# Kernel tuning notes

Measured on AMD Instinct MI355X. Metric: run time of the kernel, lower is better.

The kernel has to match this reference:

```python
import jax, jax.numpy as jnp
import numpy as np


def setup_inputs() -> dict:
    key = jax.random.key(0)
    kq, kk, kv = jax.random.split(key, 3)
    B, H, S, D = 4, 16, 2048, 64
    Q = jax.random.normal(kq, (B, H, S, D), dtype=jnp.float32)
    K = jax.random.normal(kk, (B, H, S, D), dtype=jnp.float32)
    V = jax.random.normal(kv, (B, H, S, D), dtype=jnp.float32)
    return {"Q": Q, "K": K, "V": V}


def reference(Q, K, V):
    # Faithful to the source: scale = d**(-2); scores = (Q @ K^T) / scale
    # i.e. scores are MULTIPLIED by d^2 (quirk of the original module).
    d = K.shape[-1]
    scale = jnp.asarray(d, Q.dtype) ** (-2)
    scores = jnp.einsum('bhqd,bhkd->bhqk', Q, K) / scale  # [B,H,S,S]
    attn = jax.nn.softmax(scores, axis=-1)
    out = jnp.einsum('bhqk,bhkd->bhqd', attn, V)
    return out
```

## Files before the change

kernel.cpp:

```cpp
#include <hip/hip_runtime.h>
#include <math.h>


#define S_LEN 2048
#define D_DIM 64
#define NH 64
#define BM 128
#define BN 64
#define QTILES (S_LEN / BM)
#define KTILES (S_LEN / BN)

typedef unsigned short u16;
typedef unsigned int u32;
typedef _Float16 f16;
typedef __attribute__((ext_vector_type(8))) _Float16 f16x8;
typedef __attribute__((ext_vector_type(4))) float f32x4;

#define SC_FULL (4096.0f * 1.4426950408889634f)
#define QSCALE (SC_FULL / 64.0f)
#define KSCALE 64.0f

union f16cv { f16 h; u16 u; };

__device__ __forceinline__ void split2h(float a, u16& hi, u16& lo) {
  f16cv ch, cl;
  ch.h = (f16)a;
  float r = a - (float)ch.h;
  cl.h = (f16)r;
  hi = ch.u; lo = cl.u;
}

__device__ __forceinline__ int swz(int row, int chunk) {
  return (row << 6) + ((chunk ^ (row & 7)) << 3);
}

__global__ void k_split_kernel(const float* __restrict__ K,
                               u16* __restrict__ Kh, u16* __restrict__ Km) {
  size_t i4 = ((size_t)blockIdx.x * 256 + threadIdx.x) * 4;
  float4 v = *(const float4*)(K + i4);
  u16 h0, l0, h1, l1, h2, l2, h3, l3;
  split2h(v.x * KSCALE, h0, l0);
  split2h(v.y * KSCALE, h1, l1);
  split2h(v.z * KSCALE, h2, l2);
  split2h(v.w * KSCALE, h3, l3);
  *(uint2*)(Kh + i4) = make_uint2((u32)h0 | ((u32)h1 << 16), (u32)h2 | ((u32)h3 << 16));
  *(uint2*)(Km + i4) = make_uint2((u32)l0 | ((u32)l1 << 16), (u32)l2 | ((u32)l3 << 16));
}

__global__ void v_prep_kernel(const float* __restrict__ V, u16* __restrict__ Vt) {
  __shared__ float Vf[64 * 65];
  const int tid = threadIdx.x;
  const int kt = blockIdx.x, h = blockIdx.y;
  const float* V0 = V + ((size_t)h * S_LEN + kt * 64) * 64;
  const int tx = tid & 15, ty = tid >> 4;
#pragma unroll
  for (int p = 0; p < 4; ++p) {
    int r = ty + 16 * p;
    float4 v = *(const float4*)(V0 + r * 64 + tx * 4);
    Vf[r * 65 + 4 * tx + 0] = v.x;
    Vf[r * 65 + 4 * tx + 1] = v.y;
    Vf[r * 65 + 4 * tx + 2] = v.z;
    Vf[r * 65 + 4 * tx + 3] = v.w;
  }
  __syncthreads();
  const int ch = tid & 7, dr = tid >> 3;
#pragma unroll
  for (int p = 0; p < 2; ++p) {
    int d = dr + 32 * p;
    u32 w[4];
#pragma unroll
    for (int i = 0; i < 4; ++i) {
      f16cv a, b;
      a.h = (f16)Vf[(8 * ch + 2 * i) * 65 + d];
      b.h = (f16)Vf[(8 * ch + 2 * i + 1) * 65 + d];
      w[i] = (u32)a.u | ((u32)b.u << 16);
    }
    size_t o = ((size_t)h * 64 + d) * S_LEN + (size_t)kt * 64 + 8 * ch;
    *(uint4*)(Vt + o) = make_uint4(w[0], w[1], w[2], w[3]);
  }
}

#define K0_B 0
#define K1_B 4096
#define VT_B 8192
#define P_B  12288
#define LDS_USH 20480

__global__ __launch_bounds__(512, 4)
void attn_mfma_f16(const float* __restrict__ Q, const u16* __restrict__ Kh,
                   const u16* __restrict__ Km, const u16* __restrict__ Vt,
                   float* __restrict__ O) {
  __shared__ __align__(16) u16 lds[LDS_USH];

  const int tid = threadIdx.x;
  const int lane = tid & 63;
  const int wv = tid >> 6;
  const int c = lane & 15;
  const int g = lane >> 4;
  const int h = blockIdx.x;
  const int qtile = blockIdx.y;

  f16x8 aqh[2], aqm[2];
  {
    int qrow = qtile * BM + wv * 16 + c;
    const float* qp = Q + ((size_t)h * S_LEN + qrow) * 64 + g * 8;
#pragma unroll
    for (int ks = 0; ks < 2; ++ks) {
      float4 a = *(const float4*)(qp + ks * 32);
      float4 b = *(const float4*)(qp + ks * 32 + 4);
      float v[8] = {a.x, a.y, a.z, a.w, b.x, b.y, b.z, b.w};
      f16x8 hi, lo;
#pragma unroll
      for (int e = 0; e < 8; ++e) {
        float q = v[e] * QSCALE;
        f16 qh = (f16)q;
        hi[e] = qh;
        lo[e] = (f16)(q - (float)qh);
      }
      aqh[ks] = hi; aqm[ks] = lo;
    }
  }

  f32x4 Oacc[4];
  f32x4 mrow = (f32x4){-INFINITY, -INFINITY, -INFINITY, -INFINITY};
  f32x4 lrow = (f32x4){0.f, 0.f, 0.f, 0.f};
#pragma unroll
  for (int t = 0; t < 4; ++t) Oacc[t] = (f32x4){0.f, 0.f, 0.f, 0.f};

  const int srow = tid >> 3;
  const int schk = tid & 7;
  const int sdst = swz(srow, schk);
  const size_t gKbase = ((size_t)h * S_LEN) * 64 + (size_t)srow * 64 + schk * 8;
  const size_t gVbase = (size_t)h * 64 * S_LEN + (size_t)srow * S_LEN + schk * 8;

  uint4 rkh, rkm, rvt;
  rkh = *(const uint4*)(Kh + gKbase);
  rkm = *(const uint4*)(Km + gKbase);
  rvt = *(const uint4*)(Vt + gVbase);

  for (int kt = 0; kt < KTILES; ++kt) {
    __syncthreads();
    *(uint4*)&lds[K0_B + sdst] = rkh;
    *(uint4*)&lds[K1_B + sdst] = rkm;
    *(uint4*)&lds[VT_B + sdst] = rvt;
    __syncthreads();

    if (kt + 1 < KTILES) {
      size_t gK = gKbase + (size_t)(kt + 1) * BN * 64;
      size_t gV = gVbase + (size_t)(kt + 1) * BN;
      rkh = *(const uint4*)(Kh + gK);
      rkm = *(const uint4*)(Km + gK);
      rvt = *(const uint4*)(Vt + gV);
    }

    f32x4 S[4];
#pragma unroll
    for (int t = 0; t < 4; ++t) S[t] = (f32x4){0.f, 0.f, 0.f, 0.f};
#pragma unroll
    for (int ks = 0; ks < 2; ++ks) {
#pragma unroll
      for (int t = 0; t < 4; ++t) {
        int off = swz(16 * t + c, g + 4 * ks);
        f16x8 bh = *(const f16x8*)&lds[K0_B + off];
        f16x8 bm = *(const f16x8*)&lds[K1_B + off];
        S[t] = __builtin_amdgcn_mfma_f32_16x16x32_f16(aqh[ks], bh, S[t], 0, 0, 0);
        S[t] = __builtin_amdgcn_mfma_f32_16x16x32_f16(aqh[ks], bm, S[t], 0, 0, 0);
        S[t] = __builtin_amdgcn_mfma_f32_16x16x32_f16(aqm[ks], bh, S[t], 0, 0, 0);
      }
    }

    f32x4 mx;
#pragma unroll
    for (int r = 0; r < 4; ++r)
      mx[r] = fmaxf(fmaxf(S[0][r], S[1][r]), fmaxf(S[2][r], S[3][r]));
#pragma unroll
    for (int r = 0; r < 4; ++r) {
      float v = mx[r];
      v = fmaxf(v, __shfl_xor(v, 1));
      v = fmaxf(v, __shfl_xor(v, 2));
      v = fmaxf(v, __shfl_xor(v, 4));
      v = fmaxf(v, __shfl_xor(v, 8));
      mx[r] = v;
    }
    f32x4 alpha;
#pragma unroll
    for (int r = 0; r < 4; ++r) {
      float mnew = fmaxf(mrow[r], mx[r]);
      alpha[r] = exp2f(mrow[r] - mnew);
      mrow[r] = mnew;
    }
#pragma unroll
    for (int t = 0; t < 4; ++t)
#pragma unroll
      for (int r = 0; r < 4; ++r) S[t][r] = exp2f(S[t][r] - mrow[r]);
#pragma unroll
    for (int r = 0; r < 4; ++r)
      lrow[r] = lrow[r] * alpha[r] + (S[0][r] + S[1][r] + S[2][r] + S[3][r]);
#pragma unroll
    for (int t = 0; t < 4; ++t)
#pragma unroll
      for (int r = 0; r < 4; ++r) Oacc[t][r] *= alpha[r];

#pragma unroll
    for (int r = 0; r < 4; ++r) {
      int rq = wv * 16 + 4 * g + r;
      int rowbase = (rq << 6);
      int rsw = rq & 7;
#pragma unroll
      for (int t = 0; t < 4; ++t) {
        f16cv cv; cv.h = (f16)S[t][r];
        int col = 16 * t + c;
        lds[P_B + rowbase + (((col >> 3) ^ rsw) << 3) + (col & 7)] = cv.u;
      }
    }

    f16x8 ap[2];
    {
      int rq = wv * 16 + c;
#pragma unroll
      for (int ks = 0; ks < 2; ++ks)
        ap[ks] = *(const f16x8*)&lds[P_B + swz(rq, g + 4 * ks)];
    }
#pragma unroll
    for (int ks = 0; ks < 2; ++ks) {
#pragma unroll
      for (int nt = 0; nt < 4; ++nt) {
        f16x8 bv = *(const f16x8*)&lds[VT_B + swz(16 * nt + c, g + 4 * ks)];
        Oacc[nt] = __builtin_amdgcn_mfma_f32_16x16x32_f16(ap[ks], bv, Oacc[nt], 0, 0, 0);
      }
    }
  }

  float inv[4];
#pragma unroll
  for (int r = 0; r < 4; ++r) {
    float l = lrow[r];
    l += __shfl_xor(l, 1);
    l += __shfl_xor(l, 2);
    l += __shfl_xor(l, 4);
    l += __shfl_xor(l, 8);
    inv[r] = 1.0f / l;
  }
#pragma unroll
  for (int nt = 0; nt < 4; ++nt)
#pragma unroll
    for (int r = 0; r < 4; ++r) {
      int row = qtile * BM + wv * 16 + 4 * g + r;
      O[((size_t)h * S_LEN + row) * 64 + 16 * nt + c] = Oacc[nt][r] * inv[r];
    }
}

#define LSTR 68
__global__ __launch_bounds__(256, 2)
void attn_fp32_kernel(const float* __restrict__ Q, const float* __restrict__ K,
                      const float* __restrict__ V, float* __restrict__ O) {
  __shared__ float Qs[64][LSTR];
  __shared__ float Ks[64][LSTR];
  __shared__ float Vs[64][LSTR];
  __shared__ float Ps[64][LSTR];
  const int tid = threadIdx.x;
  const int tx = tid & 15, ty = tid >> 4;
  const int qtile = blockIdx.x, head = blockIdx.y;
  const long hoff = (long)head * S_LEN * D_DIM;
  const float* Qp = Q + hoff + (long)qtile * 64 * D_DIM;
  const float* Kp = K + hoff;
  const float* Vp = V + hoff;
  float* Op = O + hoff + (long)qtile * 64 * D_DIM;
  {
    const int cc = tx * 4;
#pragma unroll
    for (int p = 0; p < 4; ++p) {
      const int r = ty + p * 16;
      *(float4*)(&Qs[r][cc]) = *(const float4*)(Qp + r * D_DIM + cc);
    }
  }
  float m_i[4], l_i[4];
  float4 o_acc[4];
#pragma unroll
  for (int i = 0; i < 4; ++i) {
    m_i[i] = -INFINITY; l_i[i] = 0.0f;
    o_acc[i] = make_float4(0.f, 0.f, 0.f, 0.f);
  }
  const float SCALE = 4096.0f;
  const float LOG2E = 1.4426950408889634f;
  for (int kt = 0; kt < S_LEN / 64; ++kt) {
    {
      const int cc = tx * 4;
      const float* Kt = Kp + kt * 64 * D_DIM;
      const float* Vv = Vp + kt * 64 * D_DIM;
#pragma unroll
      for (int p = 0; p < 4; ++p) {
        const int r = ty + p * 16;
        *(float4*)(&Ks[r][cc]) = *(const float4*)(Kt + r * D_DIM + cc);
        *(float4*)(&Vs[r][cc]) = *(const float4*)(Vv + r * D_DIM + cc);
      }
    }
    __syncthreads();
    float s[4][4];
#pragma unroll
    for (int i = 0; i < 4; ++i)
#pragma unroll
      for (int j = 0; j < 4; ++j) s[i][j] = 0.0f;
#pragma unroll
    for (int d = 0; d < D_DIM; d += 4) {
      float4 q4[4], k4[4];
#pragma unroll
      for (int i = 0; i < 4; ++i) q4[i] = *(const float4*)(&Qs[ty * 4 + i][d]);
#pragma unroll
      for (int j = 0; j < 4; ++j) k4[j] = *(const float4*)(&Ks[tx + 16 * j][d]);
#pragma unroll
      for (int i = 0; i < 4; ++i)
#pragma unroll
        for (int j = 0; j < 4; ++j) {
          s[i][j] += q4[i].x * k4[j].x; s[i][j] += q4[i].y * k4[j].y;
          s[i][j] += q4[i].z * k4[j].z; s[i][j] += q4[i].w * k4[j].w;
        }
    }
#pragma unroll
    for (int i = 0; i < 4; ++i) {
#pragma unroll
      for (int j = 0; j < 4; ++j) s[i][j] *= SCALE;
      float rm = fmaxf(fmaxf(s[i][0], s[i][1]), fmaxf(s[i][2], s[i][3]));
#pragma unroll
      for (int off = 8; off >= 1; off >>= 1) rm = fmaxf(rm, __shfl_xor(rm, off));
      const float mnew = fmaxf(m_i[i], rm);
      const float alpha = exp2f((m_i[i] - mnew) * LOG2E);
      float rs = 0.0f;
#pragma unroll
      for (int j = 0; j < 4; ++j) {
        const float p = exp2f((s[i][j] - mnew) * LOG2E);
        s[i][j] = p; rs += p;
      }
#pragma unroll
      for (int off = 8; off >= 1; off >>= 1) rs += __shfl_xor(rs, off);
      l_i[i] = l_i[i] * alpha + rs;
      m_i[i] = mnew;
      o_acc[i].x *= alpha; o_acc[i].y *= alpha; o_acc[i].z *= alpha; o_acc[i].w *= alpha;
      const int mm = ty * 4 + i;
      Ps[mm][tx] = s[i][0]; Ps[mm][tx + 16] = s[i][1];
      Ps[mm][tx + 32] = s[i][2]; Ps[mm][tx + 48] = s[i][3];
    }
    __syncthreads();
#pragma unroll
    for (int k = 0; k < 64; k += 4) {
      float4 p4[4], v4[4];
#pragma unroll
      for (int i = 0; i < 4; ++i) p4[i] = *(const float4*)(&Ps[ty * 4 + i][k]);
#pragma unroll
      for (int kk = 0; kk < 4; ++kk) v4[kk] = *(const float4*)(&Vs[k + kk][tx * 4]);
#pragma unroll
      for (int i = 0; i < 4; ++i) {
        o_acc[i].x += p4[i].x * v4[0].x + p4[i].y * v4[1].x + p4[i].z * v4[2].x + p4[i].w * v4[3].x;
        o_acc[i].y += p4[i].x * v4[0].y + p4[i].y * v4[1].y + p4[i].z * v4[2].y + p4[i].w * v4[3].y;
        o_acc[i].z += p4[i].x * v4[0].z + p4[i].y * v4[1].z + p4[i].z * v4[2].z + p4[i].w * v4[3].z;
        o_acc[i].w += p4[i].x * v4[0].w + p4[i].y * v4[1].w + p4[i].z * v4[2].w + p4[i].w * v4[3].w;
      }
    }
    __syncthreads();
  }
#pragma unroll
  for (int i = 0; i < 4; ++i) {
    const float inv = 1.0f / l_i[i];
    o_acc[i].x *= inv; o_acc[i].y *= inv; o_acc[i].z *= inv; o_acc[i].w *= inv;
    *(float4*)(Op + (ty * 4 + i) * D_DIM + tx * 4) = o_acc[i];
  }
}

extern "C" void kernel_launch(void* const* d_in, const int* in_sizes, int n_in,
                              void* d_out, int out_size, void* d_ws, size_t ws_size,
                              hipStream_t stream) {
  const float* Q = (const float*)d_in[0];
  const float* K = (const float*)d_in[1];
  const float* V = (const float*)d_in[2];
  float* O = (float*)d_out;

  const size_t P = (size_t)NH * S_LEN * D_DIM;
  const size_t need = 3 * P * sizeof(u16);

  if (ws_size >= need) {
    u16* w = (u16*)d_ws;
    u16 *Kh = w, *Km = w + P, *Vt = w + 2 * P;
    k_split_kernel<<<8192, 256, 0, stream>>>(K, Kh, Km);
    v_prep_kernel<<<dim3(KTILES, NH), 256, 0, stream>>>(V, Vt);
    attn_mfma_f16<<<dim3(NH, QTILES), 512, 0, stream>>>(Q, Kh, Km, Vt, O);
  } else {
    attn_fp32_kernel<<<dim3(S_LEN / 64, NH), 256, 0, stream>>>(Q, K, V, O);
  }
}
```

Baseline: 334.2 us.

## Give each wave two Q row-tiles, transpose S layout, fuse prep kernels

Each of four waves now owns 32 query rows in two 16-row MFMA tiles, so every K and V fragment read from LDS feeds two MFMAs. The Q·K MFMA operands are swapped so each lane holds one query row's scores, which turns the per-tile row max and sum into two cross-lane shuffles. P is written to LDS with packed fp16 conversions. The two preprocessing kernels are merged into one launch. The cost is more accumulator registers per thread and half the threads per block, which may lower occupancy and latency hiding.

```diff
diff --git a/kernel.cpp b/kernel.cpp
--- a/kernel.cpp
+++ b/kernel.cpp
@@ -14,6 +14,7 @@
 typedef unsigned int u32;
 typedef _Float16 f16;
 typedef __attribute__((ext_vector_type(8))) _Float16 f16x8;
+typedef __attribute__((ext_vector_type(2))) __fp16 fp16x2;
 typedef __attribute__((ext_vector_type(4))) float f32x4;
 
 #define SC_FULL (4096.0f * 1.4426950408889634f)
@@ -21,6 +22,7 @@
 #define KSCALE 64.0f
 
 union f16cv { f16 h; u16 u; };
+union pkcv { fp16x2 h; u32 u; };
 
 __device__ __forceinline__ void split2h(float a, u16& hi, u16& lo) {
   f16cv ch, cl;
@@ -34,49 +36,51 @@
   return (row << 6) + ((chunk ^ (row & 7)) << 3);
 }
 
-__global__ void k_split_kernel(const float* __restrict__ K,
-                               u16* __restrict__ Kh, u16* __restrict__ Km) {
-  size_t i4 = ((size_t)blockIdx.x * 256 + threadIdx.x) * 4;
-  float4 v = *(const float4*)(K + i4);
-  u16 h0, l0, h1, l1, h2, l2, h3, l3;
-  split2h(v.x * KSCALE, h0, l0);
-  split2h(v.y * KSCALE, h1, l1);
-  split2h(v.z * KSCALE, h2, l2);
-  split2h(v.w * KSCALE, h3, l3);
-  *(uint2*)(Kh + i4) = make_uint2((u32)h0 | ((u32)h1 << 16), (u32)h2 | ((u32)h3 << 16));
-  *(uint2*)(Km + i4) = make_uint2((u32)l0 | ((u32)l1 << 16), (u32)l2 | ((u32)l3 << 16));
-}
-
-__global__ void v_prep_kernel(const float* __restrict__ V, u16* __restrict__ Vt) {
-  __shared__ float Vf[64 * 65];
-  const int tid = threadIdx.x;
-  const int kt = blockIdx.x, h = blockIdx.y;
-  const float* V0 = V + ((size_t)h * S_LEN + kt * 64) * 64;
-  const int tx = tid & 15, ty = tid >> 4;
-#pragma unroll
-  for (int p = 0; p < 4; ++p) {
-    int r = ty + 16 * p;
-    float4 v = *(const float4*)(V0 + r * 64 + tx * 4);
-    Vf[r * 65 + 4 * tx + 0] = v.x;
-    Vf[r * 65 + 4 * tx + 1] = v.y;
-    Vf[r * 65 + 4 * tx + 2] = v.z;
-    Vf[r * 65 + 4 * tx + 3] = v.w;
-  }
-  __syncthreads();
-  const int ch = tid & 7, dr = tid >> 3;
-#pragma unroll
-  for (int p = 0; p < 2; ++p) {
-    int d = dr + 32 * p;
-    u32 w[4];
-#pragma unroll
-    for (int i = 0; i < 4; ++i) {
-      f16cv a, b;
-      a.h = (f16)Vf[(8 * ch + 2 * i) * 65 + d];
-      b.h = (f16)Vf[(8 * ch + 2 * i + 1) * 65 + d];
-      w[i] = (u32)a.u | ((u32)b.u << 16);
-    }
-    size_t o = ((size_t)h * 64 + d) * S_LEN + (size_t)kt * 64 + 8 * ch;
-    *(uint4*)(Vt + o) = make_uint4(w[0], w[1], w[2], w[3]);
+__global__ void prep_kernel(const float* __restrict__ K, const float* __restrict__ V,
+                            u16* __restrict__ Kh, u16* __restrict__ Km,
+                            u16* __restrict__ Vt) {
+  if (blockIdx.x < 8192) {
+    size_t i4 = ((size_t)blockIdx.x * 256 + threadIdx.x) * 4;
+    float4 v = *(const float4*)(K + i4);
+    u16 h0, l0, h1, l1, h2, l2, h3, l3;
+    split2h(v.x * KSCALE, h0, l0);
+    split2h(v.y * KSCALE, h1, l1);
+    split2h(v.z * KSCALE, h2, l2);
+    split2h(v.w * KSCALE, h3, l3);
+    *(uint2*)(Kh + i4) = make_uint2((u32)h0 | ((u32)h1 << 16), (u32)h2 | ((u32)h3 << 16));
+    *(uint2*)(Km + i4) = make_uint2((u32)l0 | ((u32)l1 << 16), (u32)l2 | ((u32)l3 << 16));
+  } else {
+    __shared__ float Vf[64 * 65];
+    const int idx = blockIdx.x - 8192;
+    const int kt = idx & 31, h = idx >> 5;
+    const int tid = threadIdx.x;
+    const float* V0 = V + ((size_t)h * S_LEN + kt * 64) * 64;
+    const int tx = tid & 15, ty = tid >> 4;
+#pragma unroll
+    for (int p = 0; p < 4; ++p) {
+      int r = ty + 16 * p;
+      float4 v = *(const float4*)(V0 + r * 64 + tx * 4);
+      Vf[r * 65 + 4 * tx + 0] = v.x;
+      Vf[r * 65 + 4 * tx + 1] = v.y;
+      Vf[r * 65 + 4 * tx + 2] = v.z;
+      Vf[r * 65 + 4 * tx + 3] = v.w;
+    }
+    __syncthreads();
+    const int ch = tid & 7, dr = tid >> 3;
+#pragma unroll
+    for (int p = 0; p < 2; ++p) {
+      int d = dr + 32 * p;
+      u32 w[4];
+#pragma unroll
+      for (int i = 0; i < 4; ++i) {
+        f16cv a, b;
+        a.h = (f16)Vf[(8 * ch + 2 * i) * 65 + d];
+        b.h = (f16)Vf[(8 * ch + 2 * i + 1) * 65 + d];
+        w[i] = (u32)a.u | ((u32)b.u << 16);
+      }
+      size_t o = ((size_t)h * 64 + d) * S_LEN + (size_t)kt * 64 + 8 * ch;
+      *(uint4*)(Vt + o) = make_uint4(w[0], w[1], w[2], w[3]);
+    }
   }
 }
 
@@ -86,7 +90,7 @@
 #define P_B  12288
 #define LDS_USH 20480
 
-__global__ __launch_bounds__(512, 4)
+__global__ __launch_bounds__(256, 3)
 void attn_mfma_f16(const float* __restrict__ Q, const u16* __restrict__ Kh,
                    const u16* __restrict__ Km, const u16* __restrict__ Vt,
                    float* __restrict__ O) {
@@ -100,9 +104,10 @@
   const int h = blockIdx.x;
   const int qtile = blockIdx.y;
 
-  f16x8 aqh[2], aqm[2];
-  {
-    int qrow = qtile * BM + wv * 16 + c;
+  f16x8 aqh[2][2], aqm[2][2];
+#pragma unroll
+  for (int m = 0; m < 2; ++m) {
+    int qrow = qtile * BM + wv * 32 + m * 16 + c;
     const float* qp = Q + ((size_t)h * S_LEN + qrow) * 64 + g * 8;
 #pragma unroll
     for (int ks = 0; ks < 2; ++ks) {
@@ -117,45 +122,57 @@
         hi[e] = qh;
         lo[e] = (f16)(q - (float)qh);
       }
-      aqh[ks] = hi; aqm[ks] = lo;
-    }
-  }
-
-  f32x4 Oacc[4];
-  f32x4 mrow = (f32x4){-INFINITY, -INFINITY, -INFINITY, -INFINITY};
-  f32x4 lrow = (f32x4){0.f, 0.f, 0.f, 0.f};
-#pragma unroll
-  for (int t = 0; t < 4; ++t) Oacc[t] = (f32x4){0.f, 0.f, 0.f, 0.f};
-
-  const int srow = tid >> 3;
-  const int schk = tid & 7;
-  const int sdst = swz(srow, schk);
-  const size_t gKbase = ((size_t)h * S_LEN) * 64 + (size_t)srow * 64 + schk * 8;
-  const size_t gVbase = (size_t)h * 64 * S_LEN + (size_t)srow * S_LEN + schk * 8;
-
-  uint4 rkh, rkm, rvt;
-  rkh = *(const uint4*)(Kh + gKbase);
-  rkm = *(const uint4*)(Km + gKbase);
-  rvt = *(const uint4*)(Vt + gVbase);
+      aqh[m][ks] = hi; aqm[m][ks] = lo;
+    }
+  }
+
+  f32x4 Oacc[2][4];
+  float mrow[2] = {-INFINITY, -INFINITY};
+  float lrow[2] = {0.f, 0.f};
+#pragma unroll
+  for (int m = 0; m < 2; ++m)
+#pragma unroll
+    for (int t = 0; t < 4; ++t) Oacc[m][t] = (f32x4){0.f, 0.f, 0.f, 0.f};
+
+  const int srow = tid >> 2;
+  const int c0 = tid & 3;
+  const int d0a = swz(srow, c0), d0b = swz(srow, c0 + 4);
+  const size_t gKbase = ((size_t)h * S_LEN + srow) * 64 + c0 * 8;
+  const size_t gVbase = ((size_t)h * 64 + srow) * S_LEN + c0 * 8;
+
+  uint4 rk0a = *(const uint4*)(Kh + gKbase);
+  uint4 rk0b = *(const uint4*)(Kh + gKbase + 32);
+  uint4 rk1a = *(const uint4*)(Km + gKbase);
+  uint4 rk1b = *(const uint4*)(Km + gKbase + 32);
+  uint4 rva  = *(const uint4*)(Vt + gVbase);
+  uint4 rvb  = *(const uint4*)(Vt + gVbase + 32);
 
   for (int kt = 0; kt < KTILES; ++kt) {
     __syncthreads();
-    *(uint4*)&lds[K0_B + sdst] = rkh;
-    *(uint4*)&lds[K1_B + sdst] = rkm;
-    *(uint4*)&lds[VT_B + sdst] = rvt;
+    *(uint4*)&lds[K0_B + d0a] = rk0a;
+    *(uint4*)&lds[K0_B + d0b] = rk0b;
+    *(uint4*)&lds[K1_B + d0a] = rk1a;
+    *(uint4*)&lds[K1_B + d0b] = rk1b;
+    *(uint4*)&lds[VT_B + d0a] = rva;
+    *(uint4*)&lds[VT_B + d0b] = rvb;
     __syncthreads();
 
     if (kt + 1 < KTILES) {
       size_t gK = gKbase + (size_t)(kt + 1) * BN * 64;
       size_t gV = gVbase + (size_t)(kt + 1) * BN;
-      rkh = *(const uint4*)(Kh + gK);
-      rkm = *(const uint4*)(Km + gK);
-      rvt = *(const uint4*)(Vt + gV);
-    }
-
-    f32x4 S[4];
-#pragma unroll
-    for (int t = 0; t < 4; ++t) S[t] = (f32x4){0.f, 0.f, 0.f, 0.f};
+      rk0a = *(const uint4*)(Kh + gK);
+      rk0b = *(const uint4*)(Kh + gK + 32);
+      rk1a = *(const uint4*)(Km + gK);
+      rk1b = *(const uint4*)(Km + gK + 32);
+      rva  = *(const uint4*)(Vt + gV);
+      rvb  = *(const uint4*)(Vt + gV + 32);
+    }
+
+    f32x4 S[2][4];
+#pragma unroll
+    for (int m = 0; m < 2; ++m)
+#pragma unroll
+      for (int t = 0; t < 4; ++t) S[m][t] = (f32x4){0.f, 0.f, 0.f, 0.f};
 #pragma unroll
     for (int ks = 0; ks < 2; ++ks) {
 #pragma unroll
@@ -163,91 +180,95 @@
         int off = swz(16 * t + c, g + 4 * ks);
         f16x8 bh = *(const f16x8*)&lds[K0_B + off];
         f16x8 bm = *(const f16x8*)&lds[K1_B + off];
-        S[t] = __builtin_amdgcn_mfma_f32_16x16x32_f16(aqh[ks], bh, S[t], 0, 0, 0);
-        S[t] = __builtin_amdgcn_mfma_f32_16x16x32_f16(aqh[ks], bm, S[t], 0, 0, 0);
-        S[t] = __builtin_amdgcn_mfma_f32_16x16x32_f16(aqm[ks], bh, S[t], 0, 0, 0);
-      }
-    }
-
-    f32x4 mx;
-#pragma unroll
-    for (int r = 0; r < 4; ++r)
-      mx[r] = fmaxf(fmaxf(S[0][r], S[1][r]), fmaxf(S[2][r], S[3][r]));
-#pragma unroll
-    for (int r = 0; r < 4; ++r) {
-      float v = mx[r];
-      v = fmaxf(v, __shfl_xor(v, 1));
-      v = fmaxf(v, __shfl_xor(v, 2));
-      v = fmaxf(v, __shfl_xor(v, 4));
-      v = fmaxf(v, __shfl_xor(v, 8));
-      mx[r] = v;
-    }
-    f32x4 alpha;
-#pragma unroll
-    for (int r = 0; r < 4; ++r) {
-      float mnew = fmaxf(mrow[r], mx[r]);
-      alpha[r] = exp2f(mrow[r] - mnew);
-      mrow[r] = mnew;
-    }
-#pragma unroll
-    for (int t = 0; t < 4; ++t)
-#pragma unroll
-      for (int r = 0; r < 4; ++r) S[t][r] = exp2f(S[t][r] - mrow[r]);
-#pragma unroll
-    for (int r = 0; r < 4; ++r)
-      lrow[r] = lrow[r] * alpha[r] + (S[0][r] + S[1][r] + S[2][r] + S[3][r]);
-#pragma unroll
-    for (int t = 0; t < 4; ++t)
-#pragma unroll
-      for (int r = 0; r < 4; ++r) Oacc[t][r] *= alpha[r];
-
-#pragma unroll
-    for (int r = 0; r < 4; ++r) {
-      int rq = wv * 16 + 4 * g + r;
-      int rowbase = (rq << 6);
-      int rsw = rq & 7;
+#pragma unroll
+        for (int m = 0; m < 2; ++m) {
+          S[m][t] = __builtin_amdgcn_mfma_f32_16x16x32_f16(bh, aqh[m][ks], S[m][t], 0, 0, 0);
+          S[m][t] = __builtin_amdgcn_mfma_f32_16x16x32_f16(bm, aqh[m][ks], S[m][t], 0, 0, 0);
+          S[m][t] = __builtin_amdgcn_mfma_f32_16x16x32_f16(bh, aqm[m][ks], S[m][t], 0, 0, 0);
+        }
+      }
+    }
+
+#pragma unroll
+    for (int m = 0; m < 2; ++m) {
+      float mx = S[m][0][0];
+#pragma unroll
+      for (int t = 0; t < 4; ++t)
+#pragma unroll
+        for (int r = 0; r < 4; ++r) mx = fmaxf(mx, S[m][t][r]);
+      mx = fmaxf(mx, __shfl_xor(mx, 16));
+      mx = fmaxf(mx, __shfl_xor(mx, 32));
+      float mnew = fmaxf(mrow[m], mx);
+      float a = exp2f(mrow[m] - mnew);
+      mrow[m] = mnew;
+      float ps = 0.f;
+#pragma unroll
+      for (int t = 0; t < 4; ++t)
+#pragma unroll
+        for (int r = 0; r < 4; ++r) {
+          float p = exp2f(S[m][t][r] - mnew);
+          S[m][t][r] = p;
+          ps += p;
+        }
+      lrow[m] = lrow[m] * a + ps;
+      float ab[4];
+#pragma unroll
+      for (int r = 0; r < 4; ++r) ab[r] = __shfl(a, (lane & 48) | (4 * g + r));
+#pragma unroll
+      for (int nt = 0; nt < 4; ++nt)
+#pragma unroll
+        for (int r = 0; r < 4; ++r) Oacc[m][nt][r] *= ab[r];
+      int rql = wv * 32 + m * 16 + c;
+      int rowbase = rql << 6;
+      int rs7 = c & 7;
 #pragma unroll
       for (int t = 0; t < 4; ++t) {
-        f16cv cv; cv.h = (f16)S[t][r];
-        int col = 16 * t + c;
-        lds[P_B + rowbase + (((col >> 3) ^ rsw) << 3) + (col & 7)] = cv.u;
-      }
-    }
-
-    f16x8 ap[2];
-    {
-      int rq = wv * 16 + c;
+        pkcv p01, p23;
+        p01.h = __builtin_amdgcn_cvt_pkrtz(S[m][t][0], S[m][t][1]);
+        p23.h = __builtin_amdgcn_cvt_pkrtz(S[m][t][2], S[m][t][3]);
+        int chunk = 2 * t + (g >> 1);
+        int off = rowbase + ((chunk ^ rs7) << 3) + 4 * (g & 1);
+        *(uint2*)&lds[P_B + off] = make_uint2(p01.u, p23.u);
+      }
+    }
+
+    f16x8 ap[2][2];
+#pragma unroll
+    for (int m = 0; m < 2; ++m) {
+      int rql = wv * 32 + m * 16 + c;
 #pragma unroll
       for (int ks = 0; ks < 2; ++ks)
-        ap[ks] = *(const f16x8*)&lds[P_B + swz(rq, g + 4 * ks)];
+        ap[m][ks] = *(const f16x8*)&lds[P_B + swz(rql, g + 4 * ks)];
     }
 #pragma unroll
     for (int ks = 0; ks < 2; ++ks) {
 #pragma unroll
       for (int nt = 0; nt < 4; ++nt) {
         f16x8 bv = *(const f16x8*)&lds[VT_B + swz(16 * nt + c, g + 4 * ks)];
-        Oacc[nt] = __builtin_amdgcn_mfma_f32_16x16x32_f16(ap[ks], bv, Oacc[nt], 0, 0, 0);
-      }
-    }
-  }
-
-  float inv[4];
-#pragma unroll
-  for (int r = 0; r < 4; ++r) {
-    float l = lrow[r];
-    l += __shfl_xor(l, 1);
-    l += __shfl_xor(l, 2);
-    l += __shfl_xor(l, 4);
-    l += __shfl_xor(l, 8);
-    inv[r] = 1.0f / l;
-  }
-#pragma unroll
-  for (int nt = 0; nt < 4; ++nt)
-#pragma unroll
-    for (int r = 0; r < 4; ++r) {
-      int row = qtile * BM + wv * 16 + 4 * g + r;
-      O[((size_t)h * S_LEN + row) * 64 + 16 * nt + c] = Oacc[nt][r] * inv[r];
-    }
+#pragma unroll
+        for (int m = 0; m < 2; ++m)
+          Oacc[m][nt] = __builtin_amdgcn_mfma_f32_16x16x32_f16(ap[m][ks], bv, Oacc[m][nt], 0, 0, 0);
+      }
+    }
+  }
+
+#pragma unroll
+  for (int m = 0; m < 2; ++m) {
+    float l = lrow[m];
+    l += __shfl_xor(l, 16);
+    l += __shfl_xor(l, 32);
+    float linv = 1.0f / l;
+    float lr[4];
+#pragma unroll
+    for (int r = 0; r < 4; ++r) lr[r] = __shfl(linv, (lane & 48) | (4 * g + r));
+#pragma unroll
+    for (int nt = 0; nt < 4; ++nt)
+#pragma unroll
+      for (int r = 0; r < 4; ++r) {
+        int row = qtile * BM + wv * 32 + m * 16 + 4 * g + r;
+        O[((size_t)h * S_LEN + row) * 64 + 16 * nt + c] = Oacc[m][nt][r] * lr[r];
+      }
+  }
 }
 
 #define LSTR 68
@@ -380,9 +401,8 @@
   if (ws_size >= need) {
     u16* w = (u16*)d_ws;
     u16 *Kh = w, *Km = w + P, *Vt = w + 2 * P;
-    k_split_kernel<<<8192, 256, 0, stream>>>(K, Kh, Km);
-    v_prep_kernel<<<dim3(KTILES, NH), 256, 0, stream>>>(V, Vt);
-    attn_mfma_f16<<<dim3(NH, QTILES), 512, 0, stream>>>(Q, Kh, Km, Vt, O);
+    prep_kernel<<<8192 + 2048, 256, 0, stream>>>(K, V, Kh, Km, Vt);
+    attn_mfma_f16<<<dim3(NH, QTILES), 256, 0, stream>>>(Q, Kh, Km, Vt, O);
   } else {
     attn_fp32_kernel<<<dim3(S_LEN / 64, NH), 256, 0, stream>>>(Q, K, V, O);
   }
```

New measurement: 300.1 us. 10.2% less time.
